# Kernel tuning notes

Measured on AMD Instinct MI355X. Metric: run time of the kernel, lower is better.

The kernel has to match this reference:

```python
import jax, jax.numpy as jnp
import numpy as np

B, S, D, H = 2, 2048, 1024, 16
HD = D // H
EPS = 1e-5


def setup_inputs() -> dict:
    key = jax.random.key(0)
    ks = jax.random.split(key, 12)
    s = 1.0 / np.sqrt(D)
    inp = {
        "q": jax.random.normal(ks[0], (B, S, D), jnp.float32),
        "k": jax.random.normal(ks[1], (B, S, D), jnp.float32),
        "v": jax.random.normal(ks[2], (B, S, D), jnp.float32),
        "mask": jnp.ones((B, S, S), jnp.int32),
        "Wq": jax.random.normal(ks[3], (D, D), jnp.float32) * s,
        "bq": jnp.zeros((D,), jnp.float32),
        "Wk": jax.random.normal(ks[4], (D, D), jnp.float32) * s,
        "bk": jnp.zeros((D,), jnp.float32),
        "Wv": jax.random.normal(ks[5], (D, D), jnp.float32) * s,
        "bv": jnp.zeros((D,), jnp.float32),
        "Wo": jax.random.normal(ks[6], (D, D), jnp.float32) * s,
        "bo": jnp.zeros((D,), jnp.float32),
        "gamma": jnp.ones((D,), jnp.float32),
        "beta": jnp.zeros((D,), jnp.float32),
    }
    return inp


def reference(q, k, v, mask, Wq, bq, Wk, bk, Wv, bv, Wo, bo, gamma, beta):
    residual = q
    # projections (torch Linear: x @ W.T + b)
    qh = (q @ Wq.T + bq).reshape(B, S, H, HD).transpose(0, 2, 1, 3)  # b h s d
    kh = (k @ Wk.T + bk).reshape(B, S, H, HD).transpose(0, 2, 1, 3)
    vh = (v @ Wv.T + bv).reshape(B, S, H, HD).transpose(0, 2, 1, 3)
    scores = jnp.einsum('bhid,bhjd->bhij', qh, kh) / jnp.sqrt(jnp.float32(HD))
    scores = jnp.where(mask[:, None, :, :] == 0, jnp.float32(-1e9), scores)
    attention = jax.nn.softmax(scores, axis=-1)  # dropout=0 (eval)
    context = jnp.einsum('bhij,bhjd->bhid', attention, vh)
    context = context.transpose(0, 2, 1, 3).reshape(B, S, D)
    out = context @ Wo.T + bo
    x = out + residual
    mu = jnp.mean(x, axis=-1, keepdims=True)
    var = jnp.mean(jnp.square(x - mu), axis=-1, keepdims=True)
    output = (x - mu) * jax.lax.rsqrt(var + EPS) * gamma + beta
    return (output, attention)
```

## Files before the change

kernel.cpp:

```cpp
#include <hip/hip_runtime.h>
#include <hip/hip_bf16.h>


typedef float f32x4 __attribute__((ext_vector_type(4)));
typedef short short8 __attribute__((ext_vector_type(8)));

#if __has_builtin(__builtin_amdgcn_exp2f)
#define EXP2(x) __builtin_amdgcn_exp2f(x)
#else
#define EXP2(x) exp2f(x)
#endif

#define QSCALE 0.18033688011112042f
#define MASKNEG -1.4426950408889634e9f

__device__ __forceinline__ short f2bs(float f) {
  union { __hip_bfloat16 h; short s; } u;
  u.h = __float2bfloat16(f);
  return u.s;
}

__device__ __forceinline__ void async16(const void* g, void* l) {
  __builtin_amdgcn_global_load_lds(
      (const __attribute__((address_space(1))) unsigned int*)g,
      (__attribute__((address_space(3))) unsigned int*)l, 16, 0, 0);
}

__global__ __launch_bounds__(256) void cvt_mask_kernel(
    const float* __restrict__ q, const float* __restrict__ k, const float* __restrict__ v,
    const float* __restrict__ wq, const float* __restrict__ wk, const float* __restrict__ wv,
    const float* __restrict__ wo, short* __restrict__ dst,
    const int* __restrict__ mask, unsigned* __restrict__ bits, unsigned* __restrict__ flags) {
  if (blockIdx.x < 8192) {
    long base = (long)blockIdx.x * 2048;
    const float* src;
    if      (base <  4194304) src = q  + base;
    else if (base <  8388608) src = k  + (base - 4194304);
    else if (base < 12582912) src = v  + (base - 8388608);
    else if (base < 13631488) src = wq + (base - 12582912);
    else if (base < 14680064) src = wk + (base - 13631488);
    else if (base < 15728640) src = wv + (base - 14680064);
    else                      src = wo + (base - 15728640);
    int off = threadIdx.x * 8;
    float4 a = *(const float4*)(src + off);
    float4 b = *(const float4*)(src + off + 4);
    short8 o;
    o[0] = f2bs(a.x); o[1] = f2bs(a.y); o[2] = f2bs(a.z); o[3] = f2bs(a.w);
    o[4] = f2bs(b.x); o[5] = f2bs(b.y); o[6] = f2bs(b.z); o[7] = f2bs(b.w);
    *(short8*)(dst + base + off) = o;
  } else {
    int bid = blockIdx.x - 8192;
    int t = threadIdx.x, w = t >> 6, lane = t & 63;
    for (int it = 0; it < 16; ++it) {
      long gw = (long)it * 8192 + bid * 4 + w;
      long base = gw * 64;
      int mv = mask[base + lane];
      unsigned long long m = __ballot(mv != 0);
      if (lane == 0)  bits[gw * 2]     = (unsigned)m;
      if (lane == 32) bits[gw * 2 + 1] = (unsigned)(m >> 32);
      if (lane == 0 && m != 0xFFFFFFFFFFFFFFFFull) {
        long j = base & 2047, i = (base >> 11) & 2047, b = base >> 22;
        atomicOr(&flags[(int)(b * 256 + (i >> 7) * 16 + (j >> 7))], 1u);
      }
    }
  }
}

__global__ __launch_bounds__(256, 2) void proj_kernel(
    const short* __restrict__ Abase, const short* __restrict__ Wbase,
    const float* __restrict__ bq, const float* __restrict__ bk, const float* __restrict__ bv,
    short* __restrict__ Qh, short* __restrict__ Kh, short* __restrict__ Vt) {
  __shared__ __align__(16) short As[2][128 * 64];
  __shared__ __align__(16) short Bs[2][128 * 64];
  const int mode = blockIdx.z;
  const short* A = Abase + (size_t)mode * 4194304;
  const short* W = Wbase + (size_t)mode * 1048576;
  const float* bias = (mode == 0) ? bq : (mode == 1 ? bk : bv);
  const int t = threadIdx.x, w = t >> 6, lane = t & 63, g = lane >> 4, lc = lane & 15;
  const int wrow = (w >> 1) * 64, wcol = (w & 1) * 64;
  const int m0 = blockIdx.x * 128, n0 = blockIdx.y * 128;

#define PSTAGE(buf, k0)                                                                     \
  do {                                                                                      \
    _Pragma("unroll") for (int i_ = 0; i_ < 4; i_++) {                                      \
      int cb = i_ * 256 + w * 64, ch = cb + lane, row = ch >> 3, c = ch & 7;                \
      int so = ((c ^ (row & 7)) << 3);                                                      \
      async16(A + (size_t)(m0 + row) * 1024 + (k0) + so, (void*)&As[buf][cb << 3]);         \
      async16(W + (size_t)(n0 + row) * 1024 + (k0) + so, (void*)&Bs[buf][cb << 3]);         \
    }                                                                                       \
  } while (0)

  f32x4 acc[4][4] = {};
  PSTAGE(0, 0);
  __syncthreads();
  int pb = 0;
  for (int kt = 0; kt < 16; ++kt) {
    if (kt < 15) PSTAGE(pb ^ 1, (kt + 1) * 64);
#pragma unroll
    for (int kf = 0; kf < 2; ++kf) {
      short8 af[4], bf[4];
#pragma unroll
      for (int m = 0; m < 4; m++) {
        int row = wrow + m * 16 + lc;
        af[m] = *(const short8*)&As[pb][(row << 6) + (((kf * 4 + g) ^ (row & 7)) << 3)];
      }
#pragma unroll
      for (int n = 0; n < 4; n++) {
        int row = wcol + n * 16 + lc;
        bf[n] = *(const short8*)&Bs[pb][(row << 6) + (((kf * 4 + g) ^ (row & 7)) << 3)];
      }
      __builtin_amdgcn_s_setprio(1);
#pragma unroll
      for (int m = 0; m < 4; m++)
#pragma unroll
        for (int n = 0; n < 4; n++)
          acc[m][n] = __builtin_amdgcn_mfma_f32_16x16x32_bf16(af[m], bf[n], acc[m][n], 0, 0, 0);
      __builtin_amdgcn_s_setprio(0);
    }
    __syncthreads();
    pb ^= 1;
  }
#undef PSTAGE
#pragma unroll
  for (int n = 0; n < 4; n++) {
    const int col = n0 + wcol + n * 16 + lc;
    const float bv_ = bias[col];
    const int h = col >> 6, d = col & 63;
#pragma unroll
    for (int m = 0; m < 4; m++)
#pragma unroll
      for (int r = 0; r < 4; r++) {
        const int srow = m0 + wrow + m * 16 + g * 4 + r;
        const int b = srow >> 11, s = srow & 2047;
        float val = acc[m][n][r] + bv_;
        if (mode == 0)
          Qh[((size_t)(b * 16 + h) * 2048 + s) * 64 + d] = f2bs(val * QSCALE);
        else if (mode == 1)
          Kh[((size_t)(b * 16 + h) * 2048 + s) * 64 + d] = f2bs(val);
        else
          Vt[((size_t)(b * 16 + h) * 64 + d) * 2048 + s] = f2bs(val);
      }
  }
}

__global__ __launch_bounds__(256, 2) void attn_kernel(
    const short* __restrict__ Qh, const short* __restrict__ Kh, const short* __restrict__ Vt,
    const unsigned* __restrict__ mbits, const unsigned* __restrict__ mflags,
    float* __restrict__ Pout, short* __restrict__ ctx) {
  __shared__ __align__(16) short Ks[2][128 * 64];
  __shared__ __align__(16) short Vs[64 * 128];
  __shared__ __align__(16) short Ps[128 * 128];
  const int L = blockIdx.x;
  const int xcd = L & 7, idx = L >> 3;
  const int bh = xcd + ((idx >> 4) << 3);
  const int qb = idx & 15;
  const int b = bh >> 4, h = bh & 15;
  const int t = threadIdx.x, w = t >> 6, lane = t & 63, g = lane >> 4, lc = lane & 15;
  const short* Qp = Qh + (size_t)bh * 2048 * 64;
  const short* Kp = Kh + (size_t)bh * 2048 * 64;
  const short* Vp = Vt + (size_t)bh * 64 * 2048;
  float* Pb = Pout + ((size_t)bh * 2048 + qb * 128) * 2048;

  short8 qf[2][2];
#pragma unroll
  for (int qm = 0; qm < 2; qm++)
#pragma unroll
    for (int kf = 0; kf < 2; kf++)
      qf[qm][kf] = *(const short8*)(Qp + (size_t)(qb * 128 + w * 32 + qm * 16 + lc) * 64 + kf * 32 + g * 8);

#define STAGE_K(buf, j0)                                                                   \
  do {                                                                                     \
    _Pragma("unroll") for (int i_ = 0; i_ < 4; i_++) {                                     \
      int cb = i_ * 256 + w * 64, ch = cb + lane, row = ch >> 3, c = ch & 7;               \
      int sc = c ^ (row & 7) ^ ((row >> 3) & 7);                                           \
      async16(Kp + (size_t)((j0) + row) * 64 + (sc << 3), (void*)&Ks[buf][cb << 3]);       \
    }                                                                                      \
  } while (0)
#define STAGE_V(j0)                                                                        \
  do {                                                                                     \
    _Pragma("unroll") for (int i_ = 0; i_ < 4; i_++) {                                     \
      int cb = i_ * 256 + w * 64, ch = cb + lane, row = ch >> 4, c = ch & 15;              \
      async16(Vp + (size_t)row * 2048 + (j0) + ((c ^ (row & 15)) << 3), (void*)&Vs[cb << 3]); \
    }                                                                                      \
  } while (0)

  float lsum[2] = {0.f, 0.f};
  int kb = 0;
  STAGE_K(0, 0);
  __syncthreads();
  for (int it = 0; it < 16; ++it) {
    if (it < 15) STAGE_K(kb ^ 1, (it + 1) * 128);
    f32x4 acc[2][8] = {};
    __builtin_amdgcn_s_setprio(1);
#pragma unroll
    for (int kf = 0; kf < 2; kf++)
#pragma unroll
      for (int n = 0; n < 8; n++) {
        int row = n * 16 + lc;
        int sc = (kf * 4 + g) ^ (row & 7) ^ ((row >> 3) & 7);
        short8 kfr = *(const short8*)&Ks[kb][(row << 6) + (sc << 3)];
        acc[0][n] = __builtin_amdgcn_mfma_f32_16x16x32_bf16(kfr, qf[0][kf], acc[0][n], 0, 0, 0);
        acc[1][n] = __builtin_amdgcn_mfma_f32_16x16x32_bf16(kfr, qf[1][kf], acc[1][n], 0, 0, 0);
      }
    __builtin_amdgcn_s_setprio(0);
    unsigned flg = mflags[b * 256 + qb * 16 + it];
    if (flg) {
#pragma unroll
      for (int qm = 0; qm < 2; qm++) {
        int ig = qb * 128 + w * 32 + qm * 16 + lc;
        uint4 mw = *(const uint4*)(mbits + ((size_t)b * 2048 + ig) * 64 + it * 4);
#pragma unroll
        for (int n = 0; n < 8; n++) {
          unsigned bw = (n >> 1) == 0 ? mw.x : ((n >> 1) == 1 ? mw.y : ((n >> 1) == 2 ? mw.z : mw.w));
#pragma unroll
          for (int r = 0; r < 4; r++)
            if (!((bw >> (((n & 1) << 4) + g * 4 + r)) & 1u)) acc[qm][n][r] = MASKNEG;
        }
      }
    }
#pragma unroll
    for (int qm = 0; qm < 2; qm++) {
      float s_ = 0.f;
#pragma unroll
      for (int n = 0; n < 8; n++)
#pragma unroll
        for (int r = 0; r < 4; r++) s_ += EXP2(acc[qm][n][r]);
      s_ += __shfl_xor(s_, 16);
      s_ += __shfl_xor(s_, 32);
      lsum[qm] += s_;
    }
    __syncthreads();
    kb ^= 1;
  }
  float* ls = (float*)Vs;
  if (g == 0) { ls[w * 32 + lc] = lsum[0]; ls[w * 32 + 16 + lc] = lsum[1]; }
  __syncthreads();
  float linv[8];
#pragma unroll
  for (int qm = 0; qm < 2; qm++)
#pragma unroll
    for (int r = 0; r < 4; r++) linv[qm * 4 + r] = 1.0f / ls[w * 32 + qm * 16 + g * 4 + r];
  kb = 0;
  STAGE_K(0, 0);
  __syncthreads();

  f32x4 acco[2][4] = {};
  for (int it = 0; it < 16; ++it) {
    const int j0 = it * 128;
    STAGE_V(j0);
    if (it < 15) STAGE_K(kb ^ 1, j0 + 128);
    f32x4 accs[2][8] = {};
    __builtin_amdgcn_s_setprio(1);
#pragma unroll
    for (int kf = 0; kf < 2; kf++)
#pragma unroll
      for (int n = 0; n < 8; n++) {
        int row = lc * 8 + n;
        int sc = (kf * 4 + g) ^ n ^ (lc & 7);
        short8 kfr = *(const short8*)&Ks[kb][(row << 6) + (sc << 3)];
        accs[0][n] = __builtin_amdgcn_mfma_f32_16x16x32_bf16(qf[0][kf], kfr, accs[0][n], 0, 0, 0);
        accs[1][n] = __builtin_amdgcn_mfma_f32_16x16x32_bf16(qf[1][kf], kfr, accs[1][n], 0, 0, 0);
      }
    __builtin_amdgcn_s_setprio(0);
    unsigned flg = mflags[b * 256 + qb * 16 + it];
    if (flg) {
#pragma unroll
      for (int qm = 0; qm < 2; qm++)
#pragma unroll
        for (int r = 0; r < 4; r++) {
          int ig = qb * 128 + w * 32 + qm * 16 + g * 4 + r;
          uint4 mw = *(const uint4*)(mbits + ((size_t)b * 2048 + ig) * 64 + it * 4);
          unsigned w01 = (lc & 4) ? mw.y : mw.x;
          unsigned w23 = (lc & 4) ? mw.w : mw.z;
          unsigned wsel = (lc & 8) ? w23 : w01;
#pragma unroll
          for (int n = 0; n < 8; n++)
            if (!((wsel >> (((lc & 3) << 3) + n)) & 1u)) accs[qm][n][r] = MASKNEG;
        }
    }
#pragma unroll
    for (int qm = 0; qm < 2; qm++)
#pragma unroll
      for (int r = 0; r < 4; r++) {
        const float li = linv[qm * 4 + r];
        const int irow = w * 32 + qm * 16 + g * 4 + r;
        f32x4 p0, p1;
#pragma unroll
        for (int n = 0; n < 4; n++) p0[n] = EXP2(accs[qm][n][r]) * li;
#pragma unroll
        for (int n = 0; n < 4; n++) p1[n] = EXP2(accs[qm][n + 4][r]) * li;
        float* pr = Pb + (size_t)irow * 2048 + j0 + (lc << 3);
        *(f32x4*)pr = p0;
        *(f32x4*)(pr + 4) = p1;
        short8 pk;
#pragma unroll
        for (int n = 0; n < 4; n++) { pk[n] = f2bs(p0[n]); pk[n + 4] = f2bs(p1[n]); }
        *(short8*)&Ps[(irow << 7) + ((lc ^ (irow & 15)) << 3)] = pk;
      }
    __syncthreads();
    __builtin_amdgcn_s_setprio(1);
#pragma unroll
    for (int kt4 = 0; kt4 < 4; kt4++) {
      short8 pa[2];
#pragma unroll
      for (int qm = 0; qm < 2; qm++) {
        int row = w * 32 + qm * 16 + lc;
        pa[qm] = *(const short8*)&Ps[(row << 7) + ((((kt4 << 2) + g) ^ (row & 15)) << 3)];
      }
#pragma unroll
      for (int dn = 0; dn < 4; dn++) {
        int d = dn * 16 + lc;
        short8 vb_ = *(const short8*)&Vs[(d << 7) + ((((kt4 << 2) + g) ^ (d & 15)) << 3)];
        acco[0][dn] = __builtin_amdgcn_mfma_f32_16x16x32_bf16(pa[0], vb_, acco[0][dn], 0, 0, 0);
        acco[1][dn] = __builtin_amdgcn_mfma_f32_16x16x32_bf16(pa[1], vb_, acco[1][dn], 0, 0, 0);
      }
    }
    __builtin_amdgcn_s_setprio(0);
    __syncthreads();
    kb ^= 1;
  }
#pragma unroll
  for (int qm = 0; qm < 2; qm++)
#pragma unroll
    for (int dn = 0; dn < 4; dn++)
#pragma unroll
      for (int r = 0; r < 4; r++) {
        int srow = qb * 128 + w * 32 + qm * 16 + g * 4 + r;
        int col = h * 64 + dn * 16 + lc;
        ctx[(size_t)(b * 2048 + srow) * 1024 + col] = f2bs(acco[qm][dn][r]);
      }
#undef STAGE_K
#undef STAGE_V
}

__global__ __launch_bounds__(256, 2) void oproj_kernel(
    const short* __restrict__ A, const short* __restrict__ W,
    const float* __restrict__ bo, const float* __restrict__ qres, float* __restrict__ xo) {
  __shared__ __align__(16) short As[2][128 * 64];
  __shared__ __align__(16) short Bs[2][128 * 64];
  const int t = threadIdx.x, w = t >> 6, lane = t & 63, g = lane >> 4, lc = lane & 15;
  const int wrow = (w >> 1) * 64, wcol = (w & 1) * 64;
  const int m0 = blockIdx.x * 128, n0 = blockIdx.y * 128;

#define OSTAGE(buf, k0)                                                                     \
  do {                                                                                      \
    _Pragma("unroll") for (int i_ = 0; i_ < 4; i_++) {                                      \
      int cb = i_ * 256 + w * 64, ch = cb + lane, row = ch >> 3, c = ch & 7;                \
      int so = ((c ^ (row & 7)) << 3);                                                      \
      async16(A + (size_t)(m0 + row) * 1024 + (k0) + so, (void*)&As[buf][cb << 3]);         \
      async16(W + (size_t)(n0 + row) * 1024 + (k0) + so, (void*)&Bs[buf][cb << 3]);         \
    }                                                                                       \
  } while (0)

  f32x4 acc[4][4] = {};
  OSTAGE(0, 0);
  __syncthreads();
  int pb = 0;
  for (int kt = 0; kt < 16; ++kt) {
    if (kt < 15) OSTAGE(pb ^ 1, (kt + 1) * 64);
#pragma unroll
    for (int kf = 0; kf < 2; ++kf) {
      short8 af[4], bf[4];
#pragma unroll
      for (int m = 0; m < 4; m++) {
        int row = wrow + m * 16 + lc;
        af[m] = *(const short8*)&As[pb][(row << 6) + (((kf * 4 + g) ^ (row & 7)) << 3)];
      }
#pragma unroll
      for (int n = 0; n < 4; n++) {
        int row = wcol + n * 16 + lc;
        bf[n] = *(const short8*)&Bs[pb][(row << 6) + (((kf * 4 + g) ^ (row & 7)) << 3)];
      }
      __builtin_amdgcn_s_setprio(1);
#pragma unroll
      for (int m = 0; m < 4; m++)
#pragma unroll
        for (int n = 0; n < 4; n++)
          acc[m][n] = __builtin_amdgcn_mfma_f32_16x16x32_bf16(af[m], bf[n], acc[m][n], 0, 0, 0);
      __builtin_amdgcn_s_setprio(0);
    }
    __syncthreads();
    pb ^= 1;
  }
#undef OSTAGE
#pragma unroll
  for (int n = 0; n < 4; n++) {
    const int col = n0 + wcol + n * 16 + lc;
    const float bv_ = bo[col];
#pragma unroll
    for (int m = 0; m < 4; m++)
#pragma unroll
      for (int r = 0; r < 4; r++) {
        const int srow = m0 + wrow + m * 16 + g * 4 + r;
        size_t o = (size_t)srow * 1024 + col;
        xo[o] = acc[m][n][r] + bv_ + qres[o];
      }
  }
}

__global__ __launch_bounds__(256) void ln_kernel(const float* __restrict__ x,
                                                 const float* __restrict__ gamma,
                                                 const float* __restrict__ beta,
                                                 float* __restrict__ out) {
  const int row = blockIdx.x, t = threadIdx.x;
  const float4 v = ((const float4*)(x + (size_t)row * 1024))[t];
  float s = v.x + v.y + v.z + v.w;
  float sq = v.x * v.x + v.y * v.y + v.z * v.z + v.w * v.w;
#pragma unroll
  for (int off = 1; off < 64; off <<= 1) { s += __shfl_xor(s, off); sq += __shfl_xor(sq, off); }
  __shared__ float ss[4], sqs[4];
  const int w = t >> 6, lane = t & 63;
  if (lane == 0) { ss[w] = s; sqs[w] = sq; }
  __syncthreads();
  s = ss[0] + ss[1] + ss[2] + ss[3];
  sq = sqs[0] + sqs[1] + sqs[2] + sqs[3];
  const float mu = s * (1.f / 1024.f);
  const float var = sq * (1.f / 1024.f) - mu * mu;
  const float rs = rsqrtf(var + 1e-5f);
  const float4 gm = ((const float4*)gamma)[t];
  const float4 bt = ((const float4*)beta)[t];
  float4 o;
  o.x = (v.x - mu) * rs * gm.x + bt.x;
  o.y = (v.y - mu) * rs * gm.y + bt.y;
  o.z = (v.z - mu) * rs * gm.z + bt.z;
  o.w = (v.w - mu) * rs * gm.w + bt.w;
  ((float4*)(out + (size_t)row * 1024))[t] = o;
}

extern "C" void kernel_launch(void* const* d_in, const int* in_sizes, int n_in,
                              void* d_out, int out_size, void* d_ws, size_t ws_size,
                              hipStream_t stream) {
  (void)in_sizes; (void)n_in; (void)out_size; (void)ws_size;
  const float* q     = (const float*)d_in[0];
  const float* k     = (const float*)d_in[1];
  const float* v     = (const float*)d_in[2];
  const int*   mask  = (const int*)d_in[3];
  const float* Wq    = (const float*)d_in[4];
  const float* bq    = (const float*)d_in[5];
  const float* Wk    = (const float*)d_in[6];
  const float* bk    = (const float*)d_in[7];
  const float* Wv    = (const float*)d_in[8];
  const float* bv    = (const float*)d_in[9];
  const float* Wo    = (const float*)d_in[10];
  const float* bo    = (const float*)d_in[11];
  const float* gamma = (const float*)d_in[12];
  const float* beta  = (const float*)d_in[13];

  char* ws = (char*)d_ws;
  short* cvtdst = (short*)ws;
  short* Qh     = (short*)(ws + 33554432);
  short* Kh     = (short*)(ws + 41943040);
  short* Vt     = (short*)(ws + 50331648);
  unsigned* mbits  = (unsigned*)(ws + 58720256);
  unsigned* mflags = (unsigned*)(ws + 59768832);
  float* x   = (float*)ws;
  short* ctx = (short*)(ws + 16777216);

  float* outln = (float*)d_out;
  float* Pout  = (float*)d_out + 4194304;

  hipMemsetAsync(mflags, 0, 2048, stream);
  cvt_mask_kernel<<<10240, 256, 0, stream>>>(q, k, v, Wq, Wk, Wv, Wo, cvtdst, mask, mbits, mflags);
  proj_kernel<<<dim3(32, 8, 3), 256, 0, stream>>>(cvtdst, cvtdst + 12582912, bq, bk, bv, Qh, Kh, Vt);
  attn_kernel<<<512, 256, 0, stream>>>(Qh, Kh, Vt, mbits, mflags, Pout, ctx);
  oproj_kernel<<<dim3(32, 8), 256, 0, stream>>>(ctx, cvtdst + 15728640, bo, q, x);
  ln_kernel<<<4096, 256, 0, stream>>>(x, gamma, beta, outln);
}
```

Before: 282.3 us.

## Read K and V fragments directly from global memory instead of LDS staging

Removes the double-buffered LDS staging of K and V tiles in the attention kernel. The MFMA fragments now load straight from global memory. Because each wave reads and writes only its own rows of the P buffer, the block-wide barriers are dropped as well. This cuts LDS footprint and synchronisation, which may allow more overlap with the large Pout stores. In exchange, each wave refetches the whole K/V tile through the caches without the swizzled bank-friendly layout, and global-load latency is no longer hidden by async prefetch.

```diff
diff --git a/kernel.cpp b/kernel.cpp
--- a/kernel.cpp
+++ b/kernel.cpp
@@ -147,9 +147,8 @@
     const short* __restrict__ Qh, const short* __restrict__ Kh, const short* __restrict__ Vt,
     const unsigned* __restrict__ mbits, const unsigned* __restrict__ mflags,
     float* __restrict__ Pout, short* __restrict__ ctx) {
-  __shared__ __align__(16) short Ks[2][128 * 64];
-  __shared__ __align__(16) short Vs[64 * 128];
   __shared__ __align__(16) short Ps[128 * 128];
+  __shared__ float ls[128];
   const int L = blockIdx.x;
   const int xcd = L & 7, idx = L >> 3;
   const int bh = xcd + ((idx >> 4) << 3);
@@ -168,37 +167,16 @@
     for (int kf = 0; kf < 2; kf++)
       qf[qm][kf] = *(const short8*)(Qp + (size_t)(qb * 128 + w * 32 + qm * 16 + lc) * 64 + kf * 32 + g * 8);
 
-#define STAGE_K(buf, j0)                                                                   \
-  do {                                                                                     \
-    _Pragma("unroll") for (int i_ = 0; i_ < 4; i_++) {                                     \
-      int cb = i_ * 256 + w * 64, ch = cb + lane, row = ch >> 3, c = ch & 7;               \
-      int sc = c ^ (row & 7) ^ ((row >> 3) & 7);                                           \
-      async16(Kp + (size_t)((j0) + row) * 64 + (sc << 3), (void*)&Ks[buf][cb << 3]);       \
-    }                                                                                      \
-  } while (0)
-#define STAGE_V(j0)                                                                        \
-  do {                                                                                     \
-    _Pragma("unroll") for (int i_ = 0; i_ < 4; i_++) {                                     \
-      int cb = i_ * 256 + w * 64, ch = cb + lane, row = ch >> 4, c = ch & 15;              \
-      async16(Vp + (size_t)row * 2048 + (j0) + ((c ^ (row & 15)) << 3), (void*)&Vs[cb << 3]); \
-    }                                                                                      \
-  } while (0)
-
   float lsum[2] = {0.f, 0.f};
-  int kb = 0;
-  STAGE_K(0, 0);
-  __syncthreads();
   for (int it = 0; it < 16; ++it) {
-    if (it < 15) STAGE_K(kb ^ 1, (it + 1) * 128);
+    const int j0 = it * 128;
     f32x4 acc[2][8] = {};
     __builtin_amdgcn_s_setprio(1);
 #pragma unroll
     for (int kf = 0; kf < 2; kf++)
 #pragma unroll
       for (int n = 0; n < 8; n++) {
-        int row = n * 16 + lc;
-        int sc = (kf * 4 + g) ^ (row & 7) ^ ((row >> 3) & 7);
-        short8 kfr = *(const short8*)&Ks[kb][(row << 6) + (sc << 3)];
+        short8 kfr = *(const short8*)(Kp + (size_t)(j0 + n * 16 + lc) * 64 + kf * 32 + g * 8);
         acc[0][n] = __builtin_amdgcn_mfma_f32_16x16x32_bf16(kfr, qf[0][kf], acc[0][n], 0, 0, 0);
         acc[1][n] = __builtin_amdgcn_mfma_f32_16x16x32_bf16(kfr, qf[1][kf], acc[1][n], 0, 0, 0);
       }
@@ -229,10 +207,7 @@
       s_ += __shfl_xor(s_, 32);
       lsum[qm] += s_;
     }
-    __syncthreads();
-    kb ^= 1;
-  }
-  float* ls = (float*)Vs;
+  }
   if (g == 0) { ls[w * 32 + lc] = lsum[0]; ls[w * 32 + 16 + lc] = lsum[1]; }
   __syncthreads();
   float linv[8];
@@ -240,24 +215,18 @@
   for (int qm = 0; qm < 2; qm++)
 #pragma unroll
     for (int r = 0; r < 4; r++) linv[qm * 4 + r] = 1.0f / ls[w * 32 + qm * 16 + g * 4 + r];
-  kb = 0;
-  STAGE_K(0, 0);
   __syncthreads();
 
   f32x4 acco[2][4] = {};
   for (int it = 0; it < 16; ++it) {
     const int j0 = it * 128;
-    STAGE_V(j0);
-    if (it < 15) STAGE_K(kb ^ 1, j0 + 128);
     f32x4 accs[2][8] = {};
     __builtin_amdgcn_s_setprio(1);
 #pragma unroll
     for (int kf = 0; kf < 2; kf++)
 #pragma unroll
       for (int n = 0; n < 8; n++) {
-        int row = lc * 8 + n;
-        int sc = (kf * 4 + g) ^ n ^ (lc & 7);
-        short8 kfr = *(const short8*)&Ks[kb][(row << 6) + (sc << 3)];
+        short8 kfr = *(const short8*)(Kp + (size_t)(j0 + lc * 8 + n) * 64 + kf * 32 + g * 8);
         accs[0][n] = __builtin_amdgcn_mfma_f32_16x16x32_bf16(qf[0][kf], kfr, accs[0][n], 0, 0, 0);
         accs[1][n] = __builtin_amdgcn_mfma_f32_16x16x32_bf16(qf[1][kf], kfr, accs[1][n], 0, 0, 0);
       }
@@ -297,7 +266,6 @@
         for (int n = 0; n < 4; n++) { pk[n] = f2bs(p0[n]); pk[n + 4] = f2bs(p1[n]); }
         *(short8*)&Ps[(irow << 7) + ((lc ^ (irow & 15)) << 3)] = pk;
       }
-    __syncthreads();
     __builtin_amdgcn_s_setprio(1);
 #pragma unroll
     for (int kt4 = 0; kt4 < 4; kt4++) {
@@ -309,15 +277,12 @@
       }
 #pragma unroll
       for (int dn = 0; dn < 4; dn++) {
-        int d = dn * 16 + lc;
-        short8 vb_ = *(const short8*)&Vs[(d << 7) + ((((kt4 << 2) + g) ^ (d & 15)) << 3)];
+        short8 vb_ = *(const short8*)(Vp + (size_t)(dn * 16 + lc) * 2048 + j0 + ((kt4 << 2) + g) * 8);
         acco[0][dn] = __builtin_amdgcn_mfma_f32_16x16x32_bf16(pa[0], vb_, acco[0][dn], 0, 0, 0);
         acco[1][dn] = __builtin_amdgcn_mfma_f32_16x16x32_bf16(pa[1], vb_, acco[1][dn], 0, 0, 0);
       }
     }
     __builtin_amdgcn_s_setprio(0);
-    __syncthreads();
-    kb ^= 1;
   }
 #pragma unroll
   for (int qm = 0; qm < 2; qm++)
@@ -329,8 +294,6 @@
         int col = h * 64 + dn * 16 + lc;
         ctx[(size_t)(b * 2048 + srow) * 1024 + col] = f2bs(acco[qm][dn][r]);
       }
-#undef STAGE_K
-#undef STAGE_V
 }
 
 __global__ __launch_bounds__(256, 2) void oproj_kernel(
```

Result: slower. 413.3 us (+46.4%).
